# Performance work log

Hardware: AMD Instinct MI355X
Metric: run time of the kernel (lower is better)

## Reference

```python
import jax, jax.numpy as jnp
import numpy as np
import math

B, T, I, H, W = 4096, 24, 128, 512, 32


def setup_inputs() -> dict:
    key = jax.random.key(0)
    ks = jax.random.split(key, 32)
    stdv = 1.0 / math.sqrt(H)
    u = lambda k, shape: jax.random.uniform(k, shape, jnp.float32, -stdv, stdv)
    inp = {
        'x_input': jax.random.normal(ks[0], (B, T, I), jnp.float32),
        'x_weather': jax.random.normal(ks[1], (B, T, W), jnp.float32),
        'w_rx': u(ks[2], (H, I)), 'w_rh': u(ks[3], (H, H)), 'w_re': u(ks[4], (H, H)), 'b_r': u(ks[5], (H, 1)),
        'w_zx': u(ks[6], (H, I)), 'w_zh': u(ks[7], (H, H)), 'w_ze': u(ks[8], (H, H)), 'b_z': u(ks[9], (H, 1)),
        'w_hx': u(ks[10], (H, I)), 'w_hh': u(ks[11], (H, H)), 'b_h': u(ks[12], (H, 1)),
        'w_d': u(ks[13], (H, I)), 'w_w': u(ks[14], (H, I)), 'w_m': u(ks[15], (H, I)),
        'w_t': u(ks[16], (H, H)), 'w_e': u(ks[17], (H, W)), 'b_e': u(ks[18], (H, 1)),
    }
    return inp


def _shift_days(x, k):
    # x: [B,T,I]; prepend k zero-days (history unavailable for first k days)
    pad = jnp.zeros((k,) + x.shape[1:], x.dtype)
    return jnp.concatenate([pad, x[:-k]], axis=0)


def _forward(x_input, x_weather, w_rx, w_rh, w_re, b_r, w_zx, w_zh, w_ze, b_z,
             w_hx, w_hh, b_h, w_d, w_w, w_m, w_t, w_e, b_e):
    h_d = _shift_days(x_input, 1)
    h_w = _shift_days(x_input, 7)
    h_m = _shift_days(x_input, 30)
    # precompute all input-only projections: [B,T,H]
    pre_o = (jnp.einsum('bti,hi->bth', h_d, w_d)
             + jnp.einsum('bti,hi->bth', h_w, w_w)
             + jnp.einsum('bti,hi->bth', h_m, w_m))
    e = jax.nn.sigmoid(jnp.einsum('btw,hw->bth', x_weather, w_e) + b_e[:, 0])
    pre_r = jnp.einsum('bti,hi->bth', x_input, w_rx) + jnp.einsum('bth,gh->btg', e, w_re) + b_r[:, 0]
    pre_z = jnp.einsum('bti,hi->bth', x_input, w_zx) + jnp.einsum('bth,gh->btg', e, w_ze) + b_z[:, 0]
    pre_h = jnp.einsum('bti,hi->bth', x_input, w_hx) + b_h[:, 0]

    def step(h_t, xs_t):
        po, pr, pz, ph = xs_t  # each [B,H]
        h_o = jax.nn.sigmoid(po + h_t @ w_t.T)
        r = jax.nn.sigmoid(pr + h_o @ w_rh.T)
        z = jax.nn.sigmoid(pz + h_o @ w_zh.T)
        h_tilde = jnp.tanh(ph + (r * h_o) @ w_hh.T)
        h_next = (1.0 - z) * h_o + z * h_tilde
        return h_next, h_next

    h0 = jnp.zeros((x_input.shape[0], w_t.shape[0]), x_input.dtype)
    xs = tuple(a.transpose(1, 0, 2) for a in (pre_o, pre_r, pre_z, pre_h))  # [T,B,H]
    _, hs = jax.lax.scan(step, h0, xs)
    return hs.transpose(1, 0, 2)  # [B,T,H]


def reference(x_input, x_weather, w_rx, w_rh, w_re, b_r, w_zx, w_zh, w_ze, b_z,
              w_hx, w_hh, b_h, w_d, w_w, w_m, w_t, w_e, b_e):
    return _forward(x_input, x_weather, w_rx, w_rh, w_re, b_r, w_zx, w_zh, w_ze, b_z,
                    w_hx, w_hh, b_h, w_d, w_w, w_m, w_t, w_e, b_e)
```

## Files before the change

kernel.cpp:

```cpp
#include <hip/hip_runtime.h>
#include <stdint.h>

#define Bsz 4096
#define Tsz 24
#define Isz 128
#define Hsz 512
#define Wsz 32
#define Msz (Bsz * Tsz)

typedef __attribute__((ext_vector_type(8))) short short8;
typedef __attribute__((ext_vector_type(4))) float f32x4;
typedef unsigned short u16;

__device__ __forceinline__ float bf2f(u16 u) {
    union { unsigned int i; float f; } v; v.i = ((unsigned int)u) << 16; return v.f;
}
__device__ __forceinline__ u16 f2bf(float f) {
    union { float f; unsigned int i; } v; v.f = f;
    unsigned int r = v.i + 0x7fffu + ((v.i >> 16) & 1u);
    return (u16)(r >> 16);
}
__device__ __forceinline__ float sigm(float x) { return 1.0f / (1.0f + expf(-x)); }

__device__ __forceinline__ f32x4 MF(short8 a, short8 b, f32x4 c) {
    return __builtin_amdgcn_mfma_f32_16x16x32_bf16(a, b, c, 0, 0, 0);
}
__device__ __forceinline__ short8 ntload8(const u16* p) {
    return __builtin_nontemporal_load((const short8*)p);
}

#define GLOAD_LDS16(SRC, DST) \
    __builtin_amdgcn_global_load_lds( \
        (__attribute__((address_space(1))) void*)(SRC), \
        (__attribute__((address_space(3))) void*)(DST), 16, 0, 0)

__global__ __launch_bounds__(256) void convert_big(
    const float* __restrict__ src, u16* __restrict__ dst, int n)
{
    int i = (blockIdx.x * 256 + threadIdx.x) * 4;
    if (i + 4 <= n) {
        float4 v = *(const float4*)(src + i);
        dst[i + 0] = f2bf(v.x); dst[i + 1] = f2bf(v.y);
        dst[i + 2] = f2bf(v.z); dst[i + 3] = f2bf(v.w);
    }
}

struct ConvDesc { const float* src; u16* dst; int n; };
struct ConvTab { ConvDesc d[13]; };

__global__ __launch_bounds__(256) void convert_many(ConvTab tab)
{
    ConvDesc cd = tab.d[blockIdx.y];
    for (int i = (blockIdx.x * 256 + threadIdx.x) * 4; i < cd.n;
         i += gridDim.x * 256 * 4) {
        float4 v = *(const float4*)(cd.src + i);
        cd.dst[i + 0] = f2bf(v.x); cd.dst[i + 1] = f2bf(v.y);
        cd.dst[i + 2] = f2bf(v.z); cd.dst[i + 3] = f2bf(v.w);
    }
}

struct Seg { const u16* A; int astr; int shift; const u16* W; int wstr; int nkb; };

__device__ __forceinline__ void stage_half(
    u16* ldsT, const u16* gbase, int rstr, int rvf,
    const u16* zerobuf, int wid, int lane)
{
#pragma unroll
    for (int q = 0; q < 4; ++q) {
        int c   = wid * 4 + q;
        int lin = c * 64 + lane;
        int row = lin >> 3;
        int gc  = lin & 7;
        const u16* src = (row >= rvf)
            ? (gbase + (long)row * rstr + ((gc ^ (row & 7)) << 3))
            : zerobuf;
        GLOAD_LDS16(src, ldsT + c * 512);
    }
}

__device__ __forceinline__ void stage_step(
    const Seg* segs, int nseg, int kb, u16* ldsA, u16* ldsB,
    int m0, int n0, const u16* zerobuf, int wid, int lane)
{
    Seg s = segs[0];
    int kloc = kb;
    if (nseg > 1 && kloc >= s.nkb) {
        kloc -= s.nkb; s = segs[1];
        if (nseg > 2 && kloc >= s.nkb) { kloc -= s.nkb; s = segs[2]; }
    }
    int base_row = m0 + s.shift;
    int rvf = base_row < 0 ? -base_row : 0;
    stage_half(ldsA, s.A + (long)base_row * s.astr + kloc * 64, s.astr, rvf,
               zerobuf, wid, lane);
    stage_half(ldsB, s.W + (long)n0 * s.wstr + kloc * 64, s.wstr, 0,
               zerobuf, wid, lane);
}

__device__ __forceinline__ void compute_tile(
    f32x4 acc[4][4], const u16* Ab, const u16* Bb, int wr, int wc, int lane)
{
    const int l15 = lane & 15;
    const int hi = lane >> 4;
#pragma unroll
    for (int ks = 0; ks < 2; ++ks) {
        int kg = ks * 4 + hi;
        short8 a[4], b[4];
#pragma unroll
        for (int am = 0; am < 4; ++am) {
            int row = wr * 64 + am * 16 + l15;
            a[am] = *(const short8*)(Ab + row * 64 + ((kg ^ (row & 7)) << 3));
        }
#pragma unroll
        for (int bn = 0; bn < 4; ++bn) {
            int row = wc * 64 + bn * 16 + l15;
            b[bn] = *(const short8*)(Bb + row * 64 + ((kg ^ (row & 7)) << 3));
        }
#pragma unroll
        for (int am = 0; am < 4; ++am)
#pragma unroll
            for (int bn = 0; bn < 4; ++bn)
                acc[am][bn] = MF(a[am], b[bn], acc[am][bn]);
    }
}

#define GEMM_CORE(SEGS, NSEG, M0, N0W)                                          \
    __shared__ u16 lds[2][2][128 * 64];                                         \
    const int lane = threadIdx.x & 63;                                          \
    const int wid  = threadIdx.x >> 6;                                          \
    const int wr = wid >> 1, wc = wid & 1;                                      \
    f32x4 acc[4][4];                                                            \
    _Pragma("unroll") for (int i_ = 0; i_ < 4; ++i_)                            \
    _Pragma("unroll") for (int j_ = 0; j_ < 4; ++j_)                            \
        acc[i_][j_] = f32x4{0, 0, 0, 0};                                        \
    int nkb = 0;                                                                \
    for (int s_ = 0; s_ < (NSEG); ++s_) nkb += (SEGS)[s_].nkb;                  \
    stage_step((SEGS), (NSEG), 0, lds[0][0], lds[0][1], (M0), (N0W),            \
               zerobuf, wid, lane);                                             \
    int cur = 0;                                                                \
    for (int kb = 0; kb < nkb; ++kb) {                                          \
        __syncthreads();                                                        \
        if (kb + 1 < nkb)                                                       \
            stage_step((SEGS), (NSEG), kb + 1, lds[cur ^ 1][0],                 \
                       lds[cur ^ 1][1], (M0), (N0W), zerobuf, wid, lane);       \
        compute_tile(acc, lds[cur][0], lds[cur][1], wr, wc, lane);              \
        cur ^= 1;                                                               \
    }

__global__ __launch_bounds__(256) void ekernel(
    const u16* __restrict__ xw, const u16* __restrict__ w_e,
    const float* __restrict__ b_e, u16* __restrict__ eout)
{
    const int lane = threadIdx.x & 63;
    const int wid  = threadIdx.x >> 6;
    const int m0 = blockIdx.x * 64 + (wid >> 1) * 32;
    const int n0 = blockIdx.y * 64 + (wid & 1) * 32;
    f32x4 acc[2][2];
    acc[0][0] = f32x4{0,0,0,0}; acc[0][1] = f32x4{0,0,0,0};
    acc[1][0] = f32x4{0,0,0,0}; acc[1][1] = f32x4{0,0,0,0};
    const int l15 = lane & 15;
    const int klane = (lane >> 4) * 8;
    short8 b0 = *(const short8*)(w_e + (n0 + l15) * Wsz + klane);
    short8 b1 = *(const short8*)(w_e + (n0 + 16 + l15) * Wsz + klane);
#pragma unroll
    for (int am = 0; am < 2; ++am) {
        short8 a = *(const short8*)(xw + (long)(m0 + am * 16 + l15) * Wsz + klane);
        acc[am][0] = MF(a, b0, acc[am][0]);
        acc[am][1] = MF(a, b1, acc[am][1]);
    }
    const int col = lane & 15;
    const int r0 = (lane >> 4) * 4;
#pragma unroll
    for (int am = 0; am < 2; ++am)
#pragma unroll
        for (int bn = 0; bn < 2; ++bn)
#pragma unroll
            for (int i = 0; i < 4; ++i) {
                long row = m0 + am * 16 + r0 + i;
                int g = n0 + bn * 16 + col;
                eout[row * Hsz + g] = f2bf(sigm(acc[am][bn][i] + b_e[g]));
            }
}

__global__ __launch_bounds__(256, 2) void prepass_kernel(
    const u16* __restrict__ x, const u16* __restrict__ e,
    const u16* __restrict__ w_d, const u16* __restrict__ w_w,
    const u16* __restrict__ w_m, const u16* __restrict__ w_rx,
    const u16* __restrict__ w_re, const u16* __restrict__ w_zx,
    const u16* __restrict__ w_ze, const u16* __restrict__ w_hx,
    const float* __restrict__ b_r, const float* __restrict__ b_z,
    const float* __restrict__ b_h,
    const u16* __restrict__ zerobuf, u16* __restrict__ prep)
{
    const int m0 = blockIdx.x * 128;
    const int y = blockIdx.y;
    const int group = y >> 2;
    const int nin = (y & 3) * 128;
    Seg segs[3];
    int nseg;
    const float* bias = nullptr;
    if (group == 0) {
        segs[0] = { x, Isz, -1 * Tsz,  w_d, Isz, Isz / 64 };
        segs[1] = { x, Isz, -7 * Tsz,  w_w, Isz, Isz / 64 };
        segs[2] = { x, Isz, -30 * Tsz, w_m, Isz, Isz / 64 };
        nseg = 3;
    } else if (group == 1) {
        segs[0] = { x, Isz, 0, w_rx, Isz, Isz / 64 };
        segs[1] = { e, Hsz, 0, w_re, Hsz, Hsz / 64 };
        nseg = 2; bias = b_r;
    } else if (group == 2) {
        segs[0] = { x, Isz, 0, w_zx, Isz, Isz / 64 };
        segs[1] = { e, Hsz, 0, w_ze, Hsz, Hsz / 64 };
        nseg = 2; bias = b_z;
    } else {
        segs[0] = { x, Isz, 0, w_hx, Isz, Isz / 64 };
        nseg = 1; bias = b_h;
    }
    GEMM_CORE(segs, nseg, m0, nin)
    const int l15 = lane & 15, hi4v = (lane >> 4) * 4;
#pragma unroll
    for (int am = 0; am < 4; ++am)
#pragma unroll
        for (int bn = 0; bn < 4; ++bn) {
            int colH = nin + wc * 64 + bn * 16 + l15;
            float bv = bias ? bias[colH] : 0.0f;
            int wv = colH >> 5, ntv = (colH >> 4) & 1, l15v = colH & 15;
#pragma unroll
            for (int i = 0; i < 4; ++i) {
                long m = m0 + wr * 64 + am * 16 + hi4v + i;
                int b = (int)(m / Tsz), t = (int)(m % Tsz);
                int bblk = b >> 4, rowin = b & 15;
                int hiv = rowin >> 2, iv = rowin & 3;
                long idx = (((long)(bblk * Tsz + t) * 4 + group) * 16 + wv) * 512
                           + (hiv * 16 + l15v) * 8 + ntv * 4 + iv;
                prep[idx] = f2bf(acc[am][bn][i] + bv);
            }
        }
}

#define SROW 528

__device__ __forceinline__ int swz(int row, int col) {
    return row * SROW + ((((col >> 3) ^ (row & 7)) << 3) | (col & 7));
}

__device__ __forceinline__ void stage_chunk(
    const u16* __restrict__ Wm, int c, u16* buf, int wave, int lane)
{
    int g1 = wave * 128 + lane;
    int g2 = g1 + 64;
    GLOAD_LDS16(Wm + (g1 >> 2) * 512 + c * 32 + (g1 & 3) * 8,
                buf + wave * 1024);
    GLOAD_LDS16(Wm + (g2 >> 2) * 512 + c * 32 + (g2 & 3) * 8,
                buf + wave * 1024 + 512);
}

__device__ __forceinline__ void wpass_staged(
    f32x4 acc[2], const u16* aS, const u16* __restrict__ Wm,
    u16* wbuf0, u16* wbuf1, int n0, int l15, int hi, int wave, int lane)
{
    const int rx = l15 & 7;
    const u16* ap = aS + l15 * SROW;
    const int bo0 = ((n0 + l15) * 4 + hi) * 8;
    const int bo1 = ((n0 + 16 + l15) * 4 + hi) * 8;
    stage_chunk(Wm, 0, wbuf0, wave, lane);
#pragma unroll 1
    for (int c = 0; c < 16; ++c) {
        __syncthreads();
        u16* cur = (c & 1) ? wbuf1 : wbuf0;
        u16* nxt = (c & 1) ? wbuf0 : wbuf1;
        if (c < 15) stage_chunk(Wm, c + 1, nxt, wave, lane);
        short8 b0 = *(const short8*)(cur + bo0);
        short8 b1 = *(const short8*)(cur + bo1);
        short8 a = *(const short8*)(ap + (((c * 4 + hi) ^ rx) << 3));
        acc[0] = MF(a, b0, acc[0]);
        acc[1] = MF(a, b1, acc[1]);
    }
}

#define FOR_FRAG \
    _Pragma("unroll") for (int nt2 = 0; nt2 < 2; ++nt2) \
    _Pragma("unroll") for (int i = 0; i < 4; ++i)

__global__ __launch_bounds__(1024, 4) void rnn_kernel(
    const u16* __restrict__ prep, const u16* __restrict__ w_t_,
    const u16* __restrict__ w_rh, const u16* __restrict__ w_zh,
    const u16* __restrict__ w_hh, float* __restrict__ out)
{
    __shared__ __align__(16) u16 hS[16 * SROW];
    __shared__ __align__(16) u16 hoS[16 * SROW];
    __shared__ __align__(16) u16 rhS[16 * SROW];
    __shared__ __align__(16) u16 wbuf0[16 * 1024];
    __shared__ __align__(16) u16 wbuf1[16 * 1024];
    const int tid = threadIdx.x;
    const int lane = tid & 63;
    const int wave = tid >> 6;
    const int l15 = lane & 15, hi = lane >> 4;
    const int n0 = wave * 32;
    const long b0 = (long)blockIdx.x * 16;

    for (int i = tid * 8; i < 16 * SROW; i += 1024 * 8)
        *(short8*)(hS + i) = (short8)0;
    __syncthreads();

    const u16* pbase = prep + (long)blockIdx.x * (Tsz * 4 * 8192)
                       + wave * 512 + lane * 8;

#pragma unroll 1
    for (int t = 0; t < Tsz; ++t) {
        const u16* pt = pbase + (long)t * 4 * 8192;
        short8 po = ntload8(pt);

        f32x4 accO[2];
        accO[0] = f32x4{0,0,0,0}; accO[1] = f32x4{0,0,0,0};
        wpass_staged(accO, hS, w_t_, wbuf0, wbuf1, n0, l15, hi, wave, lane);
        float hov[2][4];
        FOR_FRAG {
            float v = sigm(accO[nt2][i] + bf2f((u16)po[nt2 * 4 + i]));
            hov[nt2][i] = v;
            hoS[swz(hi * 4 + i, n0 + nt2 * 16 + l15)] = f2bf(v);
        }

        short8 pr = ntload8(pt + 8192);
        short8 pz = ntload8(pt + 2 * 8192);
        f32x4 accR[2];
        accR[0] = f32x4{0,0,0,0}; accR[1] = f32x4{0,0,0,0};
        wpass_staged(accR, hoS, w_rh, wbuf0, wbuf1, n0, l15, hi, wave, lane);
        f32x4 accZ[2];
        accZ[0] = f32x4{0,0,0,0}; accZ[1] = f32x4{0,0,0,0};
        wpass_staged(accZ, hoS, w_zh, wbuf0, wbuf1, n0, l15, hi, wave, lane);
        float zv[2][4];
        FOR_FRAG {
            zv[nt2][i] = sigm(accZ[nt2][i] + bf2f((u16)pz[nt2 * 4 + i]));
            float rv = sigm(accR[nt2][i] + bf2f((u16)pr[nt2 * 4 + i]));
            rhS[swz(hi * 4 + i, n0 + nt2 * 16 + l15)] = f2bf(rv * hov[nt2][i]);
        }

        short8 ph = ntload8(pt + 3 * 8192);
        f32x4 accH[2];
        accH[0] = f32x4{0,0,0,0}; accH[1] = f32x4{0,0,0,0};
        wpass_staged(accH, rhS, w_hh, wbuf0, wbuf1, n0, l15, hi, wave, lane);
        FOR_FRAG {
            int row = hi * 4 + i, col = n0 + nt2 * 16 + l15;
            float htl = tanhf(accH[nt2][i] + bf2f((u16)ph[nt2 * 4 + i]));
            float z = zv[nt2][i];
            float hn = (1.0f - z) * hov[nt2][i] + z * htl;
            __builtin_nontemporal_store(
                hn, &out[((b0 + row) * Tsz + t) * (long)Hsz + col]);
            hS[swz(row, col)] = f2bf(hn);
        }
        __syncthreads();
    }
}

extern "C" void kernel_launch(void* const* d_in, const int* in_sizes, int n_in,
                              void* d_out, int out_size, void* d_ws, size_t ws_size,
                              hipStream_t stream) {
    const float* x_f    = (const float*)d_in[0];
    const float* xw_f   = (const float*)d_in[1];
    const float* w_rx_f = (const float*)d_in[2];
    const float* w_rh_f = (const float*)d_in[3];
    const float* w_re_f = (const float*)d_in[4];
    const float* b_r    = (const float*)d_in[5];
    const float* w_zx_f = (const float*)d_in[6];
    const float* w_zh_f = (const float*)d_in[7];
    const float* w_ze_f = (const float*)d_in[8];
    const float* b_z    = (const float*)d_in[9];
    const float* w_hx_f = (const float*)d_in[10];
    const float* w_hh_f = (const float*)d_in[11];
    const float* b_h    = (const float*)d_in[12];
    const float* w_d_f  = (const float*)d_in[13];
    const float* w_w_f  = (const float*)d_in[14];
    const float* w_m_f  = (const float*)d_in[15];
    const float* w_t_f  = (const float*)d_in[16];
    const float* w_e_f  = (const float*)d_in[17];
    const float* b_e    = (const float*)d_in[18];
    float* out = (float*)d_out;

    char* ws = (char*)d_ws;
    size_t off = 0;
    auto alloc = [&](size_t bytes) {
        size_t o = off; off = (off + bytes + 255) & ~(size_t)255; return o;
    };
    const size_t nx  = (size_t)Msz * Isz;
    const size_t nxw = (size_t)Msz * Wsz;

    u16* x_bf  = (u16*)(ws + alloc(nx * 2));
    u16* xw_bf = (u16*)(ws + alloc(nxw * 2));
    u16* w_rx  = (u16*)(ws + alloc(Hsz * Isz * 2));
    u16* w_rh  = (u16*)(ws + alloc(Hsz * Hsz * 2));
    u16* w_re  = (u16*)(ws + alloc(Hsz * Hsz * 2));
    u16* w_zx  = (u16*)(ws + alloc(Hsz * Isz * 2));
    u16* w_zh  = (u16*)(ws + alloc(Hsz * Hsz * 2));
    u16* w_ze  = (u16*)(ws + alloc(Hsz * Hsz * 2));
    u16* w_hx  = (u16*)(ws + alloc(Hsz * Isz * 2));
    u16* w_hh  = (u16*)(ws + alloc(Hsz * Hsz * 2));
    u16* w_d   = (u16*)(ws + alloc(Hsz * Isz * 2));
    u16* w_w   = (u16*)(ws + alloc(Hsz * Isz * 2));
    u16* w_m   = (u16*)(ws + alloc(Hsz * Isz * 2));
    u16* w_t   = (u16*)(ws + alloc(Hsz * Hsz * 2));
    u16* w_e   = (u16*)(ws + alloc(Hsz * Wsz * 2));
    u16* e_bf  = (u16*)(ws + alloc((size_t)Msz * Hsz * 2));
    u16* prep  = (u16*)(ws + alloc((size_t)Msz * 2048 * 2));
    u16* zerobuf = (u16*)(ws + alloc(256));

    convert_big<<<(int)(nx / 1024), 256, 0, stream>>>(x_f, x_bf, (int)nx);
    convert_big<<<(int)(nxw / 1024), 256, 0, stream>>>(xw_f, xw_bf, (int)nxw);
    ConvTab tab;
    tab.d[0]  = { w_rx_f, w_rx, Hsz * Isz };
    tab.d[1]  = { w_rh_f, w_rh, Hsz * Hsz };
    tab.d[2]  = { w_re_f, w_re, Hsz * Hsz };
    tab.d[3]  = { w_zx_f, w_zx, Hsz * Isz };
    tab.d[4]  = { w_zh_f, w_zh, Hsz * Hsz };
    tab.d[5]  = { w_ze_f, w_ze, Hsz * Hsz };
    tab.d[6]  = { w_hx_f, w_hx, Hsz * Isz };
    tab.d[7]  = { w_hh_f, w_hh, Hsz * Hsz };
    tab.d[8]  = { w_d_f,  w_d,  Hsz * Isz };
    tab.d[9]  = { w_w_f,  w_w,  Hsz * Isz };
    tab.d[10] = { w_m_f,  w_m,  Hsz * Isz };
    tab.d[11] = { w_t_f,  w_t,  Hsz * Hsz };
    tab.d[12] = { w_e_f,  w_e,  Hsz * Wsz };
    convert_many<<<dim3(256, 13), 256, 0, stream>>>(tab);
    hipMemsetAsync(zerobuf, 0, 256, stream);

    ekernel<<<dim3(Msz / 64, Hsz / 64), 256, 0, stream>>>(xw_bf, w_e, b_e, e_bf);

    prepass_kernel<<<dim3(Msz / 128, 16), 256, 0, stream>>>(
        x_bf, e_bf, w_d, w_w, w_m, w_rx, w_re, w_zx, w_ze, w_hx,
        b_r, b_z, b_h, zerobuf, prep);

    rnn_kernel<<<Bsz / 16, 1024, 0, stream>>>(prep, w_t, w_rh, w_zh, w_hh, out);
}
```

Measured before the change: 1.727 ms.

## Triple-buffer weight staging with XOR-swizzled LDS layout and explicit vmcnt waits

Moves the per-chunk weight staging from double to triple buffering, so chunk c+2 is fetched while chunk c is consumed. It replaces __syncthreads with an explicit s_waitcnt vmcnt(2) plus s_barrier, and fully unrolls the 16-chunk loop. The staged weights are laid out in LDS with an XOR swizzle to cut bank conflicts on the fragment reads. All four pre-activation loads are hoisted to the top of the timestep. This costs an extra 32KB LDS buffer and adds barriers between passes, which may lower occupancy.

```diff
diff --git a/kernel.cpp b/kernel.cpp
--- a/kernel.cpp
+++ b/kernel.cpp
@@ -246,35 +246,50 @@
 __device__ __forceinline__ void stage_chunk(
     const u16* __restrict__ Wm, int c, u16* buf, int wave, int lane)
 {
-    int g1 = wave * 128 + lane;
-    int g2 = g1 + 64;
-    GLOAD_LDS16(Wm + (g1 >> 2) * 512 + c * 32 + (g1 & 3) * 8,
+    int s1 = wave * 128 + lane;
+    int s2 = s1 + 64;
+    int p1 = s1 >> 3, g1 = (s1 & 7) ^ (p1 & 7);
+    int p2 = s2 >> 3, g2 = (s2 & 7) ^ (p2 & 7);
+    GLOAD_LDS16(Wm + (long)(2 * p1 + (g1 >> 2)) * 512 + c * 32 + (g1 & 3) * 8,
                 buf + wave * 1024);
-    GLOAD_LDS16(Wm + (g2 >> 2) * 512 + c * 32 + (g2 & 3) * 8,
+    GLOAD_LDS16(Wm + (long)(2 * p2 + (g2 >> 2)) * 512 + c * 32 + (g2 & 3) * 8,
                 buf + wave * 1024 + 512);
 }
+
+#define WITER(C, RB, SB, VM) { \
+    asm volatile("s_waitcnt vmcnt(" VM ")" ::: "memory"); \
+    asm volatile("s_barrier" ::: "memory"); \
+    if ((C) < 14) stage_chunk(Wm, (C) + 2, SB, wave, lane); \
+    short8 b0 = *(const short8*)((RB) + bo0); \
+    short8 b1 = *(const short8*)((RB) + bo0 + 512); \
+    short8 a = *(const short8*)(ap + ((((C) * 4 + hi) ^ rx) << 3)); \
+    acc[0] = MF(a, b0, acc[0]); \
+    acc[1] = MF(a, b1, acc[1]); }
 
 __device__ __forceinline__ void wpass_staged(
     f32x4 acc[2], const u16* aS, const u16* __restrict__ Wm,
-    u16* wbuf0, u16* wbuf1, int n0, int l15, int hi, int wave, int lane)
-{
-    const int rx = l15 & 7;
+    u16* wb0, u16* wb1, u16* wb2,
+    int bo0, int rx, int hi, int wave, int lane, int l15)
+{
     const u16* ap = aS + l15 * SROW;
-    const int bo0 = ((n0 + l15) * 4 + hi) * 8;
-    const int bo1 = ((n0 + 16 + l15) * 4 + hi) * 8;
-    stage_chunk(Wm, 0, wbuf0, wave, lane);
-#pragma unroll 1
-    for (int c = 0; c < 16; ++c) {
-        __syncthreads();
-        u16* cur = (c & 1) ? wbuf1 : wbuf0;
-        u16* nxt = (c & 1) ? wbuf0 : wbuf1;
-        if (c < 15) stage_chunk(Wm, c + 1, nxt, wave, lane);
-        short8 b0 = *(const short8*)(cur + bo0);
-        short8 b1 = *(const short8*)(cur + bo1);
-        short8 a = *(const short8*)(ap + (((c * 4 + hi) ^ rx) << 3));
-        acc[0] = MF(a, b0, acc[0]);
-        acc[1] = MF(a, b1, acc[1]);
-    }
+    stage_chunk(Wm, 0, wb0, wave, lane);
+    stage_chunk(Wm, 1, wb1, wave, lane);
+    WITER(0,  wb0, wb2, "2")
+    WITER(1,  wb1, wb0, "2")
+    WITER(2,  wb2, wb1, "2")
+    WITER(3,  wb0, wb2, "2")
+    WITER(4,  wb1, wb0, "2")
+    WITER(5,  wb2, wb1, "2")
+    WITER(6,  wb0, wb2, "2")
+    WITER(7,  wb1, wb0, "2")
+    WITER(8,  wb2, wb1, "2")
+    WITER(9,  wb0, wb2, "2")
+    WITER(10, wb1, wb0, "2")
+    WITER(11, wb2, wb1, "2")
+    WITER(12, wb0, wb2, "2")
+    WITER(13, wb1, wb0, "2")
+    WITER(14, wb2, wb1, "2")
+    WITER(15, wb0, wb2, "0")
 }
 
 #define FOR_FRAG \
@@ -291,12 +306,16 @@
     __shared__ __align__(16) u16 rhS[16 * SROW];
     __shared__ __align__(16) u16 wbuf0[16 * 1024];
     __shared__ __align__(16) u16 wbuf1[16 * 1024];
+    __shared__ __align__(16) u16 wbuf2[16 * 1024];
     const int tid = threadIdx.x;
     const int lane = tid & 63;
     const int wave = tid >> 6;
     const int l15 = lane & 15, hi = lane >> 4;
+    const int rx = l15 & 7;
     const int n0 = wave * 32;
     const long b0 = (long)blockIdx.x * 16;
+    const int bo0 = (wave * 128 + (l15 >> 1) * 8
+                     + ((hi + 4 * (l15 & 1)) ^ (l15 >> 1))) * 8;
 
     for (int i = tid * 8; i < 16 * SROW; i += 1024 * 8)
         *(short8*)(hS + i) = (short8)0;
@@ -309,36 +328,44 @@
     for (int t = 0; t < Tsz; ++t) {
         const u16* pt = pbase + (long)t * 4 * 8192;
         short8 po = ntload8(pt);
+        short8 pr = ntload8(pt + 8192);
+        short8 pz = ntload8(pt + 2 * 8192);
+        short8 ph = ntload8(pt + 3 * 8192);
 
         f32x4 accO[2];
         accO[0] = f32x4{0,0,0,0}; accO[1] = f32x4{0,0,0,0};
-        wpass_staged(accO, hS, w_t_, wbuf0, wbuf1, n0, l15, hi, wave, lane);
+        wpass_staged(accO, hS, w_t_, wbuf0, wbuf1, wbuf2,
+                     bo0, rx, hi, wave, lane, l15);
         float hov[2][4];
         FOR_FRAG {
             float v = sigm(accO[nt2][i] + bf2f((u16)po[nt2 * 4 + i]));
             hov[nt2][i] = v;
             hoS[swz(hi * 4 + i, n0 + nt2 * 16 + l15)] = f2bf(v);
         }
-
-        short8 pr = ntload8(pt + 8192);
-        short8 pz = ntload8(pt + 2 * 8192);
+        __syncthreads();
+
         f32x4 accR[2];
         accR[0] = f32x4{0,0,0,0}; accR[1] = f32x4{0,0,0,0};
-        wpass_staged(accR, hoS, w_rh, wbuf0, wbuf1, n0, l15, hi, wave, lane);
+        wpass_staged(accR, hoS, w_rh, wbuf0, wbuf1, wbuf2,
+                     bo0, rx, hi, wave, lane, l15);
+        __syncthreads();
+
         f32x4 accZ[2];
         accZ[0] = f32x4{0,0,0,0}; accZ[1] = f32x4{0,0,0,0};
-        wpass_staged(accZ, hoS, w_zh, wbuf0, wbuf1, n0, l15, hi, wave, lane);
+        wpass_staged(accZ, hoS, w_zh, wbuf0, wbuf1, wbuf2,
+                     bo0, rx, hi, wave, lane, l15);
         float zv[2][4];
         FOR_FRAG {
             zv[nt2][i] = sigm(accZ[nt2][i] + bf2f((u16)pz[nt2 * 4 + i]));
             float rv = sigm(accR[nt2][i] + bf2f((u16)pr[nt2 * 4 + i]));
             rhS[swz(hi * 4 + i, n0 + nt2 * 16 + l15)] = f2bf(rv * hov[nt2][i]);
         }
-
-        short8 ph = ntload8(pt + 3 * 8192);
+        __syncthreads();
+
         f32x4 accH[2];
         accH[0] = f32x4{0,0,0,0}; accH[1] = f32x4{0,0,0,0};
-        wpass_staged(accH, rhS, w_hh, wbuf0, wbuf1, n0, l15, hi, wave, lane);
+        wpass_staged(accH, rhS, w_hh, wbuf0, wbuf1, wbuf2,
+                     bo0, rx, hi, wave, lane, l15);
         FOR_FRAG {
             int row = hi * 4 + i, col = n0 + nt2 * 16 + l15;
             float htl = tanhf(accH[nt2][i] + bf2f((u16)ph[nt2 * 4 + i]));
```

Result: slower. 3.433 ms (+98.8%).
